# Performance work log

Measured on AMD Instinct MI355X. Metric: run time of the kernel, lower is better.

The kernel has to match this reference:

```python
import math
import jax, jax.numpy as jnp
import numpy as np

N, C, T, V = 32, 256, 128, 25
DK, DV, NH = 64, 256, 8
DKH, DVH = DK // NH, DV // NH
EPS = 1e-5


def _spatial_pe(channels, joints):
    # spatial positional encoding: position = joint index, same for all frames
    pos = jnp.arange(joints, dtype=jnp.float32)  # (V,)
    div = jnp.exp(jnp.arange(0, channels, 2, dtype=jnp.float32) * (-math.log(10000.0) / channels))
    ang = pos[:, None] * div[None, :]  # (V, C/2)
    pe = jnp.stack([jnp.sin(ang), jnp.cos(ang)], axis=-1).reshape(joints, channels)  # interleave sin/cos
    return pe.T  # (C, V)


def _qkv_heads(inp, qkv_w, qkv_b):
    # inp: (N, T, C, V); 1x1 conv == channel GEMM
    qkv = jnp.einsum('oc,ntcv->ntov', qkv_w, inp) + qkv_b[None, None, :, None]
    q = qkv[:, :, :DK].reshape(N, T, NH, DKH, V) * (DKH ** -0.5)
    k = qkv[:, :, DK:2 * DK].reshape(N, T, NH, DKH, V)
    g = qkv[:, :, 2 * DK:3 * DK].reshape(N, T, NH, DKH, V)
    v = qkv[:, :, 3 * DK:].reshape(N, T, NH, DVH, V)
    return q, k, g, v


def setup_inputs() -> dict:
    key = jax.random.key(0)
    ks = jax.random.split(key, 3)
    return {
        'x': jax.random.normal(ks[0], (N, C, T, V), dtype=jnp.float32),
        'qkv_w': jax.random.normal(ks[1], (3 * DK + DV, C), dtype=jnp.float32) * 0.02,
        'qkv_b': jnp.zeros((3 * DK + DV,), dtype=jnp.float32),
        'attn_w': jax.random.normal(ks[2], (DV, DV), dtype=jnp.float32) * 0.02,
        'attn_b': jnp.zeros((DV,), dtype=jnp.float32),
        'dbn_gamma': jnp.ones((C * V,), dtype=jnp.float32),
        'dbn_beta': jnp.zeros((C * V,), dtype=jnp.float32),
        'bn_gamma': jnp.ones((DV,), dtype=jnp.float32),
        'bn_beta': jnp.zeros((DV,), dtype=jnp.float32),
    }


def reference(x, qkv_w, qkv_b, attn_w, attn_b, dbn_gamma, dbn_beta, bn_gamma, bn_beta):
    x_sum = x
    pe = _spatial_pe(C, V)  # (C, V)
    pos = x + pe[None, :, None, :]  # broadcast over N, T

    # data_bn: BatchNorm1d over C*V features (training mode, batch stats over N and T)
    xr = x.transpose(0, 1, 3, 2).reshape(N, C * V, T)
    mu = xr.mean(axis=(0, 2))
    var = xr.var(axis=(0, 2))
    xr = (xr - mu[None, :, None]) * jax.lax.rsqrt(var + EPS)[None, :, None]
    xr = xr * dbn_gamma[None, :, None] + dbn_beta[None, :, None]
    xn = xr.reshape(N, C, V, T).transpose(0, 1, 3, 2)  # (N, C, T, V)

    xa = xn.transpose(0, 2, 1, 3)   # (N, T, C, V)
    pa = pos.transpose(0, 2, 1, 3)  # (N, T, C, V)

    q, k, g, v = _qkv_heads(xa, qkv_w, qkv_b)
    pq, pk, _, _ = _qkv_heads(pa, qkv_w, qkv_b)

    mu_q = q.mean(-1, keepdims=True)          # (N,T,Nh,dkh,1)
    qc = q - mu_q
    pairwise = jnp.einsum('nthdv,nthdw->nthvw', qc, k)    # (N,T,Nh,V,V)
    unary = jnp.einsum('nthdv,nthdw->nthvw', mu_q, g)     # (N,T,Nh,1,V)
    lp = jnp.einsum('nthdv,nthdw->nthvw', pq, pk)         # (N,T,Nh,V,V)

    weights = jnp.tanh(pairwise + lp) + jnp.tanh(unary + lp)
    attn = jnp.einsum('nthvw,nthew->nthev', weights, v)   # (N,T,Nh,dvh,V)
    attn = attn.reshape(N, T, DV, V)
    attn = jnp.einsum('oe,ntev->ntov', attn_w, attn) + attn_b[None, None, :, None]
    y = attn.transpose(0, 2, 1, 3) + x_sum  # skip (in_c == out_c)

    # bn: BatchNorm2d over out_c (training mode)
    mu2 = y.mean(axis=(0, 2, 3))
    var2 = y.var(axis=(0, 2, 3))
    y = (y - mu2[None, :, None, None]) * jax.lax.rsqrt(var2 + EPS)[None, :, None, None]
    y = y * bn_gamma[None, :, None, None] + bn_beta[None, :, None, None]
    return jax.nn.relu(y)
```

## Files before the change

kernel.cpp:

```cpp
#include <hip/hip_runtime.h>
#include <hip/hip_bf16.h>
#include <math.h>

#define N_   32
#define C_   256
#define T_   128
#define V_   25
#define CTV  (C_ * T_ * V_)
#define TV   (T_ * V_)
#define EPS_ 1e-5f
#define S_Q  0.35355339059327373f
#define NCOPY 64

typedef __attribute__((ext_vector_type(8))) short bf16x8;
typedef __attribute__((ext_vector_type(4))) float f32x4;

__device__ inline ushort f2b(float f) {
    __hip_bfloat16 h = __float2bfloat16(f);
    return *reinterpret_cast<ushort*>(&h);
}
__device__ inline float b2f(ushort u) {
    __hip_bfloat16 h;
    *reinterpret_cast<ushort*>(&h) = u;
    return __bfloat162float(h);
}
__device__ inline float tanh_fast(float x) {
    float xc = fminf(fmaxf(x, -12.f), 12.f);
    float e = __expf(xc + xc);
    return (e - 1.f) * __builtin_amdgcn_rcpf(e + 1.f);
}
#define LD8(p) (*(const bf16x8*)(p))
#define MFMA16(a, b, c) __builtin_amdgcn_mfma_f32_16x16x32_bf16(a, b, c, 0, 0, 0)

__device__ inline int qtswz(int v, int col) {
    return v * 320 + ((((col >> 3)) ^ (v & 7)) << 3) + (col & 7);
}
__device__ inline int qvswz(int e, int w) {
    return e * 32 + (((w >> 3) ^ (e & 3)) << 3) + (w & 7);
}
__device__ inline int bswz(int v, int c) {
    return v * 256 + ((((c >> 3) ^ (v & 7)) << 3) | (c & 7));
}

__global__ void prep_kernel(const float* __restrict__ qkv_w,
                            const float* __restrict__ attn_w,
                            ushort* __restrict__ Wq, ushort* __restrict__ Wa,
                            float* __restrict__ pe, float* __restrict__ bins) {
    int idx = blockIdx.x * blockDim.x + threadIdx.x;
    int stride = gridDim.x * blockDim.x;
    for (int i = idx; i < 448 * 256; i += stride) {
        float w = qkv_w[i];
        if (i < 64 * 256) w *= S_Q;
        Wq[i] = f2b(w);
    }
    for (int i = idx; i < 256 * 256; i += stride) Wa[i] = f2b(attn_w[i]);
    for (int i = idx; i < C_ * V_; i += stride) {
        int c = i / V_, v = i - c * V_;
        int j2 = c & ~1;
        float ang = (float)v * expf(-logf(10000.0f) * (float)j2 / (float)C_);
        pe[i] = (c & 1) ? cosf(ang) : sinf(ang);
    }
    for (int i = idx; i < NCOPY * 512; i += stride) bins[i] = 0.f;
}

__global__ __launch_bounds__(1024) void dbn_kernel(const float* __restrict__ x,
                                                   const float* __restrict__ gamma,
                                                   const float* __restrict__ beta,
                                                   float* __restrict__ a_scale,
                                                   float* __restrict__ a_shift) {
    __shared__ float pgS[32][25], pgQ[32][25];
    int c = blockIdx.x;
    int tid = threadIdx.x, g = tid >> 5, l = tid & 31;
    float s = 0.f, s2 = 0.f;
    if (l < 25) {
        const float* base = x + (size_t)g * CTV + c * TV + l;
        #pragma unroll 8
        for (int t = 0; t < 128; ++t) {
            float v = base[t * 25];
            s += v; s2 += v * v;
        }
        pgS[g][l] = s; pgQ[g][l] = s2;
    }
    __syncthreads();
    if (tid < 25) {
        float S = 0.f, Q = 0.f;
        #pragma unroll
        for (int g2 = 0; g2 < 32; ++g2) { S += pgS[g2][tid]; Q += pgQ[g2][tid]; }
        float inv = 1.0f / 4096.0f;
        float mean = S * inv, var = Q * inv - mean * mean;
        int f = c * 25 + tid;
        float sc = rsqrtf(var + EPS_) * gamma[f];
        a_scale[f] = sc;
        a_shift[f] = beta[f] - mean * sc;
    }
}

__global__ void mkbias_kernel(const ushort* __restrict__ Wq,
                              const float* __restrict__ qkv_b,
                              const float* __restrict__ a_shift,
                              const float* __restrict__ pe,
                              float* __restrict__ bias2, float* __restrict__ peproj) {
    int id = blockIdx.x * 256 + threadIdx.x;
    if (id < 11200) {
        int o = id / 25, v = id - o * 25;
        float acc = qkv_b[o] * (o < 64 ? S_Q : 1.f);
        for (int c = 0; c < 256; ++c)
            acc = fmaf(b2f(Wq[o * 256 + c]), a_shift[c * 25 + v], acc);
        bias2[id] = acc;
    } else if (id < 14400) {
        int id2 = id - 11200;
        int r = id2 / 25, v = id2 - r * 25;
        float acc = qkv_b[r] * (r < 64 ? S_Q : 1.f);
        for (int c = 0; c < 256; ++c)
            acc = fmaf(b2f(Wq[r * 256 + c]), pe[c * 25 + v], acc);
        peproj[id2] = acc;
    }
}

__global__ __launch_bounds__(512, 4) void fused_kernel(
        const float* __restrict__ x,
        const ushort* __restrict__ Wq,
        const float* __restrict__ bias2, const float* __restrict__ peproj,
        const float* __restrict__ a_scale,
        const ushort* __restrict__ Wa, const float* __restrict__ attn_b,
        float* __restrict__ out, float* __restrict__ bins) {
    __shared__ __align__(16) char smem[53248];
    ushort* Braw = (ushort*)smem;
    ushort* Bxn  = (ushort*)(smem + 16384);
    ushort* qkvT = (ushort*)(smem + 32768);
    ushort* qkvV = (ushort*)smem;
    ushort* aT   = (ushort*)(smem + 16384);
    ushort* pbuf = (ushort*)(smem + 32768);

    int n = blockIdx.x >> 7, t = blockIdx.x & 127;
    int tid = threadIdx.x, wave = tid >> 6, lane = tid & 63;
    int lr = lane & 15, lg = lane >> 4;
    const float* xp = x + (size_t)n * CTV + t * V_;
    float* outp = out + (size_t)n * CTV + t * V_;
    float* mybins = bins + (blockIdx.x & (NCOPY - 1)) * 512;
    const f32x4 zacc = {0.f, 0.f, 0.f, 0.f};
    const bf16x8 zero8 = {0, 0, 0, 0, 0, 0, 0, 0};

    for (int i = tid; i < 6400; i += 512) {
        int c = i / 25, v = i - c * 25;
        float xv = xp[c * TV + v];
        int off = bswz(v, c);
        Braw[off] = f2b(xv);
        Bxn[off]  = f2b(xv * a_scale[i]);
    }
    for (int i = tid; i < 1792; i += 512) {
        int v = 25 + (i >> 8), c = i & 255;
        int off = v * 256 + c;
        Braw[off] = 0; Bxn[off] = 0;
    }
    __syncthreads();

    {
        const ushort* Arow = Wq + (wave * 16 + lr) * 256;
        f32x4 a0 = zacc, a1 = zacc;
        #pragma unroll
        for (int kk = 0; kk < 8; ++kk) {
            int k0 = kk * 32 + lg * 8;
            int oct = (((k0 >> 3) ^ (lr & 7)) << 3);
            bf16x8 a  = LD8(Arow + k0);
            bf16x8 b0 = LD8(Braw + lr * 256 + oct);
            bf16x8 b1 = LD8(Braw + (16 + lr) * 256 + oct);
            a0 = MFMA16(a, b0, a0);
            a1 = MFMA16(a, b1, a1);
        }
        #pragma unroll
        for (int i2 = 0; i2 < 4; ++i2) {
            int r = wave * 16 + lg * 4 + i2;
            qkvT[qtswz(lr, 192 + r)] = f2b(a0[i2] + peproj[r * 25 + lr]);
            qkvT[qtswz(16 + lr, 192 + r)] =
                (lr < 9) ? f2b(a1[i2] + peproj[r * 25 + 16 + lr]) : (ushort)0;
        }
    }
    __syncthreads();

    {
        int myTiles = (wave < 4) ? 4 : 3;
        f32x4 acc[4][2];
        #pragma unroll
        for (int i = 0; i < 4; ++i) { acc[i][0] = zacc; acc[i][1] = zacc; }
        #pragma unroll
        for (int kk = 0; kk < 8; ++kk) {
            int k0 = kk * 32 + lg * 8;
            int oct = (((k0 >> 3) ^ (lr & 7)) << 3);
            bf16x8 b0 = LD8(Bxn + lr * 256 + oct);
            bf16x8 b1 = LD8(Bxn + (16 + lr) * 256 + oct);
            #pragma unroll
            for (int tt = 0; tt < 4; ++tt) {
                if (tt < myTiles) {
                    int mt = wave + tt * 8;
                    bf16x8 a = LD8(Wq + (mt * 16 + lr) * 256 + k0);
                    acc[tt][0] = MFMA16(a, b0, acc[tt][0]);
                    acc[tt][1] = MFMA16(a, b1, acc[tt][1]);
                }
            }
        }
        #pragma unroll
        for (int tt = 0; tt < 4; ++tt) {
            if (tt < myTiles) {
                int mt = wave + tt * 8;
                #pragma unroll
                for (int i2 = 0; i2 < 4; ++i2) {
                    int o = mt * 16 + lg * 4 + i2;
                    float v0 = acc[tt][0][i2] + bias2[o * 25 + lr];
                    float v1 = acc[tt][1][i2] + ((lr < 9) ? bias2[o * 25 + 16 + lr] : 0.f);
                    if (mt < 12) {
                        qkvT[qtswz(lr, o)] = f2b(v0);
                        qkvT[qtswz(16 + lr, o)] = (lr < 9) ? f2b(v1) : (ushort)0;
                    } else {
                        int e = o - 192;
                        qkvV[qvswz(e, lr)] = f2b(v0);
                        qkvV[qvswz(e, 16 + lr)] = (lr < 9) ? f2b(v1) : (ushort)0;
                    }
                }
            }
        }
    }
    __syncthreads();

    int h = wave;
    float qs = 0.f;
    if (lane < 8) {
        #pragma unroll
        for (int v = 0; v < 25; ++v)
            qs += b2f(qkvT[v * 320 + ((h ^ (v & 7)) << 3) + lane]);
        qs *= (1.f / 25.f);
    }
    float m[8];
    #pragma unroll
    for (int d = 0; d < 8; ++d) m[d] = __shfl(qs, d, 64);
    float u1a = 0.f, u1b = 0.f, u2a = 0.f, u2b = 0.f;
    {
        int ra = lr, rb = 16 + lr;
        int ka = ((8 + h) ^ (ra & 7)) << 3, kb = ((8 + h) ^ (rb & 7)) << 3;
        int ga = ((16 + h) ^ (ra & 7)) << 3, gb = ((16 + h) ^ (rb & 7)) << 3;
        #pragma unroll
        for (int d = 0; d < 8; ++d) {
            u1a = fmaf(m[d], b2f(qkvT[ra * 320 + ka + d]), u1a);
            u1b = fmaf(m[d], b2f(qkvT[rb * 320 + kb + d]), u1b);
            u2a = fmaf(m[d], b2f(qkvT[ra * 320 + ga + d]), u2a);
            u2b = fmaf(m[d], b2f(qkvT[rb * 320 + gb + d]), u2b);
        }
    }
    bf16x8 aP1[2], aP2[2], bP1[2], bP2[2];
    #pragma unroll
    for (int mi = 0; mi < 2; ++mi) {
        int row = mi * 16 + lr, sx = row & 7;
        const ushort* rp = qkvT + row * 320;
        aP1[mi] = (lg == 0) ? LD8(rp + ((h ^ sx) << 3))
                : (lg == 1) ? LD8(rp + (((24 + h) ^ sx) << 3)) : zero8;
        aP2[mi] = (lg == 0) ? LD8(rp + (((24 + h) ^ sx) << 3)) : zero8;
        bP1[mi] = (lg == 0) ? LD8(rp + (((8 + h) ^ sx) << 3))
                : (lg == 1) ? LD8(rp + (((32 + h) ^ sx) << 3)) : zero8;
        bP2[mi] = (lg == 0) ? LD8(rp + (((32 + h) ^ sx) << 3)) : zero8;
    }
    f32x4 p1[2][2], p2[2][2];
    #pragma unroll
    for (int mi = 0; mi < 2; ++mi)
        #pragma unroll
        for (int ni = 0; ni < 2; ++ni) {
            p1[mi][ni] = MFMA16(aP1[mi], bP1[ni], zacc);
            p2[mi][ni] = MFMA16(aP2[mi], bP2[ni], zacc);
        }
    __syncthreads();

    #pragma unroll
    for (int mi = 0; mi < 2; ++mi)
        #pragma unroll
        for (int ni = 0; ni < 2; ++ni) {
            float uu1 = ni ? u1b : u1a, uu2 = ni ? u2b : u2a;
            int w = ni * 16 + lr;
            #pragma unroll
            for (int i2 = 0; i2 < 4; ++i2) {
                int v = mi * 16 + lg * 4 + i2;
                float tw = tanh_fast(p1[mi][ni][i2] - uu1) + tanh_fast(p2[mi][ni][i2] + uu2);
                pbuf[(h * 32 + v) * 40 + w] = (w < 25) ? f2b(tw) : (ushort)0;
            }
        }

    {
        bf16x8 aw[2], bv[2];
        #pragma unroll
        for (int mi = 0; mi < 2; ++mi)
            aw[mi] = LD8(pbuf + (h * 32 + mi * 16 + lr) * 40 + lg * 8);
        #pragma unroll
        for (int ni = 0; ni < 2; ++ni) {
            int e = h * 32 + ni * 16 + lr;
            bv[ni] = LD8(qkvV + e * 32 + ((lg ^ (e & 3)) << 3));
        }
        f32x4 at_[2][2];
        #pragma unroll
        for (int mi = 0; mi < 2; ++mi)
            #pragma unroll
            for (int ni = 0; ni < 2; ++ni)
                at_[mi][ni] = MFMA16(aw[mi], bv[ni], zacc);
        #pragma unroll
        for (int mi = 0; mi < 2; ++mi)
            #pragma unroll
            for (int ni = 0; ni < 2; ++ni)
                #pragma unroll
                for (int i2 = 0; i2 < 4; ++i2) {
                    int v = mi * 16 + lg * 4 + i2;
                    int e = h * 32 + ni * 16 + lr;
                    aT[bswz(v, e)] = (v < 25) ? f2b(at_[mi][ni][i2]) : (ushort)0;
                }
    }
    __syncthreads();

    #pragma unroll
    for (int tt = 0; tt < 2; ++tt) {
        int o0 = (wave + tt * 8) * 16;
        const ushort* Arow = Wa + (o0 + lr) * 256;
        f32x4 a0 = zacc, a1 = zacc;
        #pragma unroll
        for (int kk = 0; kk < 8; ++kk) {
            int k0 = kk * 32 + lg * 8;
            int oct = (((k0 >> 3) ^ (lr & 7)) << 3);
            bf16x8 a  = LD8(Arow + k0);
            bf16x8 b0 = LD8(aT + lr * 256 + oct);
            bf16x8 b1 = LD8(aT + (16 + lr) * 256 + oct);
            a0 = MFMA16(a, b0, a0);
            a1 = MFMA16(a, b1, a1);
        }
        #pragma unroll
        for (int i2 = 0; i2 < 4; ++i2) {
            int o = o0 + lg * 4 + i2;
            float bias = attn_b[o];
            float v0 = a0[i2] + bias + xp[o * TV + lr];
            outp[o * TV + lr] = v0;
            float v1 = 0.f;
            if (lr < 9) {
                v1 = a1[i2] + bias + xp[o * TV + 16 + lr];
                outp[o * TV + 16 + lr] = v1;
            }
            float cs = v0 + v1, cq = v0 * v0 + v1 * v1;
            #pragma unroll
            for (int mm = 1; mm < 16; mm <<= 1) {
                cs += __shfl_xor(cs, mm, 64);
                cq += __shfl_xor(cq, mm, 64);
            }
            if (lr == 0) {
                atomicAdd(&mybins[o], cs);
                atomicAdd(&mybins[256 + o], cq);
            }
        }
    }
}

__global__ void bn2_final_kernel(const float* __restrict__ bins,
                                 const float* __restrict__ gamma,
                                 const float* __restrict__ beta,
                                 float* __restrict__ scale,
                                 float* __restrict__ shift) {
    int c = threadIdx.x;
    float s = 0.f, q = 0.f;
    for (int cp = 0; cp < NCOPY; ++cp) {
        s += bins[cp * 512 + c];
        q += bins[cp * 512 + 256 + c];
    }
    float inv = 1.0f / (float)(N_ * TV);
    float mean = s * inv;
    float var = q * inv - mean * mean;
    float sc = rsqrtf(var + EPS_) * gamma[c];
    scale[c] = sc;
    shift[c] = beta[c] - mean * sc;
}

__global__ void bn2_apply_kernel(float4* __restrict__ y,
                                 const float* __restrict__ scale,
                                 const float* __restrict__ shift) {
    const int total4 = N_ * CTV / 4;
    for (int i = blockIdx.x * blockDim.x + threadIdx.x; i < total4;
         i += gridDim.x * blockDim.x) {
        int c = (i / (TV / 4)) & 255;
        float4 v = y[i];
        float sc = scale[c], sh = shift[c];
        v.x = fmaxf(fmaf(v.x, sc, sh), 0.f);
        v.y = fmaxf(fmaf(v.y, sc, sh), 0.f);
        v.z = fmaxf(fmaf(v.z, sc, sh), 0.f);
        v.w = fmaxf(fmaf(v.w, sc, sh), 0.f);
        y[i] = v;
    }
}

extern "C" void kernel_launch(void* const* d_in, const int* in_sizes, int n_in,
                              void* d_out, int out_size, void* d_ws, size_t ws_size,
                              hipStream_t stream) {
    const float* x      = (const float*)d_in[0];
    const float* qkv_w  = (const float*)d_in[1];
    const float* qkv_b  = (const float*)d_in[2];
    const float* attn_w = (const float*)d_in[3];
    const float* attn_b = (const float*)d_in[4];
    const float* dbn_g  = (const float*)d_in[5];
    const float* dbn_b  = (const float*)d_in[6];
    const float* bn_g   = (const float*)d_in[7];
    const float* bn_b   = (const float*)d_in[8];
    float* out = (float*)d_out;

    char* ws = (char*)d_ws;
    ushort* Wq      = (ushort*)ws;
    ushort* Wa      = (ushort*)(ws + 229376);
    float*  pe      = (float*)(ws + 360448);
    float*  a_scale = (float*)(ws + 386048);
    float*  a_shift = (float*)(ws + 411648);
    float*  bias2   = (float*)(ws + 437248);
    float*  peproj  = (float*)(ws + 482048);
    float*  bins    = (float*)(ws + 494848);
    float*  bn2_sc  = (float*)(ws + 625920);
    float*  bn2_sh  = (float*)(ws + 626944);

    prep_kernel<<<256, 256, 0, stream>>>(qkv_w, attn_w, Wq, Wa, pe, bins);
    dbn_kernel<<<C_, 1024, 0, stream>>>(x, dbn_g, dbn_b, a_scale, a_shift);
    mkbias_kernel<<<57, 256, 0, stream>>>(Wq, qkv_b, a_shift, pe, bias2, peproj);
    fused_kernel<<<N_ * T_, 512, 0, stream>>>(x, Wq, bias2, peproj, a_scale,
                                              Wa, attn_b, out, bins);
    bn2_final_kernel<<<1, 256, 0, stream>>>(bins, bn_g, bn_b, bn2_sc, bn2_sh);
    bn2_apply_kernel<<<4096, 256, 0, stream>>>((float4*)out, bn2_sc, bn2_sh);
}
```

Before: 380.3 us.

## Fold query-mean centering and unary term into MFMA via K-extension

Computes the per-head query mean inside the QKV GEMM epilogue through a shuffle reduction plus a precomputed bias sum. The centered q is stored directly, and the mean and g vectors are packed as extra K lanes of the second pairwise MFMA, so the separate scalar mean and unary loops disappear. It also prefetches x and the scale into registers before the LDS stores, vectorizes the LDS stores, and preloads the skip-connection values before the output GEMM. This adds a tiny extra kernel and a small LDS region. Rounding the mean to bf16 slightly changes the numerics.

```diff
diff --git a/kernel.cpp b/kernel.cpp
--- a/kernel.cpp
+++ b/kernel.cpp
@@ -14,6 +14,7 @@
 
 typedef __attribute__((ext_vector_type(8))) short bf16x8;
 typedef __attribute__((ext_vector_type(4))) float f32x4;
+typedef __attribute__((ext_vector_type(4))) unsigned short u16x4;
 
 __device__ inline ushort f2b(float f) {
     __hip_bfloat16 h = __float2bfloat16(f);
@@ -117,20 +118,30 @@
     }
 }
 
+__global__ void b2sum_kernel(const float* __restrict__ bias2,
+                             float* __restrict__ bias2sum) {
+    int o = threadIdx.x;
+    float s = 0.f;
+    #pragma unroll
+    for (int v = 0; v < 25; ++v) s += bias2[o * 25 + v];
+    bias2sum[o] = s;
+}
+
 __global__ __launch_bounds__(512, 4) void fused_kernel(
         const float* __restrict__ x,
         const ushort* __restrict__ Wq,
         const float* __restrict__ bias2, const float* __restrict__ peproj,
-        const float* __restrict__ a_scale,
+        const float* __restrict__ a_scale, const float* __restrict__ bias2sum,
         const ushort* __restrict__ Wa, const float* __restrict__ attn_b,
         float* __restrict__ out, float* __restrict__ bins) {
-    __shared__ __align__(16) char smem[53248];
+    __shared__ __align__(16) char smem[53376];
     ushort* Braw = (ushort*)smem;
     ushort* Bxn  = (ushort*)(smem + 16384);
     ushort* qkvT = (ushort*)(smem + 32768);
     ushort* qkvV = (ushort*)smem;
     ushort* aT   = (ushort*)(smem + 16384);
     ushort* pbuf = (ushort*)(smem + 32768);
+    ushort* qmub = (ushort*)(smem + 53248);
 
     int n = blockIdx.x >> 7, t = blockIdx.x & 127;
     int tid = threadIdx.x, wave = tid >> 6, lane = tid & 63;
@@ -141,17 +152,40 @@
     const f32x4 zacc = {0.f, 0.f, 0.f, 0.f};
     const bf16x8 zero8 = {0, 0, 0, 0, 0, 0, 0, 0};
 
-    for (int i = tid; i < 6400; i += 512) {
-        int c = i / 25, v = i - c * 25;
-        float xv = xp[c * TV + v];
-        int off = bswz(v, c);
-        Braw[off] = f2b(xv);
-        Bxn[off]  = f2b(xv * a_scale[i]);
-    }
-    for (int i = tid; i < 1792; i += 512) {
-        int v = 25 + (i >> 8), c = i & 255;
-        int off = v * 256 + c;
-        Braw[off] = 0; Bxn[off] = 0;
+    float b2s[4] = {0.f, 0.f, 0.f, 0.f};
+    if (wave < 4) {
+        #pragma unroll
+        for (int i2 = 0; i2 < 4; ++i2)
+            b2s[i2] = bias2sum[wave * 16 + lg * 4 + i2];
+    }
+
+    {
+        float xv[13], sc[13];
+        #pragma unroll
+        for (int j = 0; j < 13; ++j) {
+            int i = tid + j * 512;
+            if (i < 6400) {
+                int c = i / 25, v = i - c * 25;
+                xv[j] = xp[c * TV + v];
+                sc[j] = a_scale[i];
+            }
+        }
+        #pragma unroll
+        for (int j = 0; j < 13; ++j) {
+            int i = tid + j * 512;
+            if (i < 6400) {
+                int c = i / 25, v = i - c * 25;
+                int off = bswz(v, c);
+                Braw[off] = f2b(xv[j]);
+                Bxn[off]  = f2b(xv[j] * sc[j]);
+            }
+        }
+        for (int i = tid; i < 448; i += 512) {
+            int v = 25 + (i >> 6), c = (i & 63) * 4;
+            u16x4 z4 = {0, 0, 0, 0};
+            *(u16x4*)(Braw + v * 256 + c) = z4;
+            *(u16x4*)(Bxn + v * 256 + c) = z4;
+        }
     }
     __syncthreads();
 
@@ -168,13 +202,16 @@
             a0 = MFMA16(a, b0, a0);
             a1 = MFMA16(a, b1, a1);
         }
+        int rb = wave * 16 + lg * 4;
+        u16x4 r0, r1;
         #pragma unroll
         for (int i2 = 0; i2 < 4; ++i2) {
-            int r = wave * 16 + lg * 4 + i2;
-            qkvT[qtswz(lr, 192 + r)] = f2b(a0[i2] + peproj[r * 25 + lr]);
-            qkvT[qtswz(16 + lr, 192 + r)] =
-                (lr < 9) ? f2b(a1[i2] + peproj[r * 25 + 16 + lr]) : (ushort)0;
-        }
+            int r = rb + i2;
+            r0[i2] = f2b(a0[i2] + peproj[r * 25 + lr]);
+            r1[i2] = (lr < 9) ? f2b(a1[i2] + peproj[r * 25 + 16 + lr]) : (ushort)0;
+        }
+        *(u16x4*)(qkvT + qtswz(lr, 192 + rb)) = r0;
+        *(u16x4*)(qkvT + qtswz(16 + lr, 192 + rb)) = r1;
     }
     __syncthreads();
 
@@ -203,18 +240,48 @@
         for (int tt = 0; tt < 4; ++tt) {
             if (tt < myTiles) {
                 int mt = wave + tt * 8;
-                #pragma unroll
-                for (int i2 = 0; i2 < 4; ++i2) {
-                    int o = mt * 16 + lg * 4 + i2;
-                    float v0 = acc[tt][0][i2] + bias2[o * 25 + lr];
-                    float v1 = acc[tt][1][i2] + ((lr < 9) ? bias2[o * 25 + 16 + lr] : 0.f);
-                    if (mt < 12) {
-                        qkvT[qtswz(lr, o)] = f2b(v0);
-                        qkvT[qtswz(16 + lr, o)] = (lr < 9) ? f2b(v1) : (ushort)0;
-                    } else {
+                int ob = mt * 16 + lg * 4;
+                if (mt < 4) {
+                    u16x4 r0, r1;
+                    #pragma unroll
+                    for (int i2 = 0; i2 < 4; ++i2) {
+                        int o = ob + i2;
+                        float cs = acc[tt][0][i2] + ((lr < 9) ? acc[tt][1][i2] : 0.f);
+                        #pragma unroll
+                        for (int mm = 1; mm < 16; mm <<= 1)
+                            cs += __shfl_xor(cs, mm, 64);
+                        float mu = (cs + b2s[i2]) * 0.04f;
+                        ushort mur = f2b(mu);
+                        float muf = b2f(mur);
+                        r0[i2] = f2b(acc[tt][0][i2] + bias2[o * 25 + lr] - muf);
+                        r1[i2] = (lr < 9)
+                            ? f2b(acc[tt][1][i2] + bias2[o * 25 + 16 + lr] - muf)
+                            : (ushort)0;
+                        if (lr == 0) qmub[o] = mur;
+                    }
+                    *(u16x4*)(qkvT + qtswz(lr, ob)) = r0;
+                    *(u16x4*)(qkvT + qtswz(16 + lr, ob)) = r1;
+                } else if (mt < 12) {
+                    u16x4 r0, r1;
+                    #pragma unroll
+                    for (int i2 = 0; i2 < 4; ++i2) {
+                        int o = ob + i2;
+                        r0[i2] = f2b(acc[tt][0][i2] + bias2[o * 25 + lr]);
+                        r1[i2] = (lr < 9)
+                            ? f2b(acc[tt][1][i2] + bias2[o * 25 + 16 + lr])
+                            : (ushort)0;
+                    }
+                    *(u16x4*)(qkvT + qtswz(lr, ob)) = r0;
+                    *(u16x4*)(qkvT + qtswz(16 + lr, ob)) = r1;
+                } else {
+                    #pragma unroll
+                    for (int i2 = 0; i2 < 4; ++i2) {
+                        int o = ob + i2;
                         int e = o - 192;
-                        qkvV[qvswz(e, lr)] = f2b(v0);
-                        qkvV[qvswz(e, 16 + lr)] = (lr < 9) ? f2b(v1) : (ushort)0;
+                        qkvV[qvswz(e, lr)] = f2b(acc[tt][0][i2] + bias2[o * 25 + lr]);
+                        qkvV[qvswz(e, 16 + lr)] = (lr < 9)
+                            ? f2b(acc[tt][1][i2] + bias2[o * 25 + 16 + lr])
+                            : (ushort)0;
                     }
                 }
             }
@@ -223,29 +290,7 @@
     __syncthreads();
 
     int h = wave;
-    float qs = 0.f;
-    if (lane < 8) {
-        #pragma unroll
-        for (int v = 0; v < 25; ++v)
-            qs += b2f(qkvT[v * 320 + ((h ^ (v & 7)) << 3) + lane]);
-        qs *= (1.f / 25.f);
-    }
-    float m[8];
-    #pragma unroll
-    for (int d = 0; d < 8; ++d) m[d] = __shfl(qs, d, 64);
-    float u1a = 0.f, u1b = 0.f, u2a = 0.f, u2b = 0.f;
-    {
-        int ra = lr, rb = 16 + lr;
-        int ka = ((8 + h) ^ (ra & 7)) << 3, kb = ((8 + h) ^ (rb & 7)) << 3;
-        int ga = ((16 + h) ^ (ra & 7)) << 3, gb = ((16 + h) ^ (rb & 7)) << 3;
-        #pragma unroll
-        for (int d = 0; d < 8; ++d) {
-            u1a = fmaf(m[d], b2f(qkvT[ra * 320 + ka + d]), u1a);
-            u1b = fmaf(m[d], b2f(qkvT[rb * 320 + kb + d]), u1b);
-            u2a = fmaf(m[d], b2f(qkvT[ra * 320 + ga + d]), u2a);
-            u2b = fmaf(m[d], b2f(qkvT[rb * 320 + gb + d]), u2b);
-        }
-    }
+    bf16x8 mu8 = LD8(qmub + h * 8);
     bf16x8 aP1[2], aP2[2], bP1[2], bP2[2];
     #pragma unroll
     for (int mi = 0; mi < 2; ++mi) {
@@ -253,10 +298,12 @@
         const ushort* rp = qkvT + row * 320;
         aP1[mi] = (lg == 0) ? LD8(rp + ((h ^ sx) << 3))
                 : (lg == 1) ? LD8(rp + (((24 + h) ^ sx) << 3)) : zero8;
-        aP2[mi] = (lg == 0) ? LD8(rp + (((24 + h) ^ sx) << 3)) : zero8;
+        aP2[mi] = (lg == 0) ? LD8(rp + (((24 + h) ^ sx) << 3))
+                : (lg == 1) ? mu8 : zero8;
         bP1[mi] = (lg == 0) ? LD8(rp + (((8 + h) ^ sx) << 3))
                 : (lg == 1) ? LD8(rp + (((32 + h) ^ sx) << 3)) : zero8;
-        bP2[mi] = (lg == 0) ? LD8(rp + (((32 + h) ^ sx) << 3)) : zero8;
+        bP2[mi] = (lg == 0) ? LD8(rp + (((32 + h) ^ sx) << 3))
+                : (lg == 1) ? LD8(rp + (((16 + h) ^ sx) << 3)) : zero8;
     }
     f32x4 p1[2][2], p2[2][2];
     #pragma unroll
@@ -272,12 +319,11 @@
     for (int mi = 0; mi < 2; ++mi)
         #pragma unroll
         for (int ni = 0; ni < 2; ++ni) {
-            float uu1 = ni ? u1b : u1a, uu2 = ni ? u2b : u2a;
             int w = ni * 16 + lr;
             #pragma unroll
             for (int i2 = 0; i2 < 4; ++i2) {
                 int v = mi * 16 + lg * 4 + i2;
-                float tw = tanh_fast(p1[mi][ni][i2] - uu1) + tanh_fast(p2[mi][ni][i2] + uu2);
+                float tw = tanh_fast(p1[mi][ni][i2]) + tanh_fast(p2[mi][ni][i2]);
                 pbuf[(h * 32 + v) * 40 + w] = (w < 25) ? f2b(tw) : (ushort)0;
             }
         }
@@ -306,11 +352,20 @@
                 for (int i2 = 0; i2 < 4; ++i2) {
                     int v = mi * 16 + lg * 4 + i2;
                     int e = h * 32 + ni * 16 + lr;
-                    aT[bswz(v, e)] = (v < 25) ? f2b(at_[mi][ni][i2]) : (ushort)0;
+                    if (v < 25) aT[bswz(v, e)] = f2b(at_[mi][ni][i2]);
                 }
     }
     __syncthreads();
 
+    float sk0[2][4], sk1[2][4];
+    #pragma unroll
+    for (int tt = 0; tt < 2; ++tt)
+        #pragma unroll
+        for (int i2 = 0; i2 < 4; ++i2) {
+            int o = (wave + tt * 8) * 16 + lg * 4 + i2;
+            sk0[tt][i2] = xp[o * TV + lr];
+            sk1[tt][i2] = (lr < 9) ? xp[o * TV + 16 + lr] : 0.f;
+        }
     #pragma unroll
     for (int tt = 0; tt < 2; ++tt) {
         int o0 = (wave + tt * 8) * 16;
@@ -330,11 +385,11 @@
         for (int i2 = 0; i2 < 4; ++i2) {
             int o = o0 + lg * 4 + i2;
             float bias = attn_b[o];
-            float v0 = a0[i2] + bias + xp[o * TV + lr];
+            float v0 = a0[i2] + bias + sk0[tt][i2];
             outp[o * TV + lr] = v0;
             float v1 = 0.f;
             if (lr < 9) {
-                v1 = a1[i2] + bias + xp[o * TV + 16 + lr];
+                v1 = a1[i2] + bias + sk1[tt][i2];
                 outp[o * TV + 16 + lr] = v1;
             }
             float cs = v0 + v1, cq = v0 * v0 + v1 * v1;
@@ -402,22 +457,24 @@
     float* out = (float*)d_out;
 
     char* ws = (char*)d_ws;
-    ushort* Wq      = (ushort*)ws;
-    ushort* Wa      = (ushort*)(ws + 229376);
-    float*  pe      = (float*)(ws + 360448);
-    float*  a_scale = (float*)(ws + 386048);
-    float*  a_shift = (float*)(ws + 411648);
-    float*  bias2   = (float*)(ws + 437248);
-    float*  peproj  = (float*)(ws + 482048);
-    float*  bins    = (float*)(ws + 494848);
-    float*  bn2_sc  = (float*)(ws + 625920);
-    float*  bn2_sh  = (float*)(ws + 626944);
+    ushort* Wq       = (ushort*)ws;
+    ushort* Wa       = (ushort*)(ws + 229376);
+    float*  pe       = (float*)(ws + 360448);
+    float*  a_scale  = (float*)(ws + 386048);
+    float*  a_shift  = (float*)(ws + 411648);
+    float*  bias2    = (float*)(ws + 437248);
+    float*  peproj   = (float*)(ws + 482048);
+    float*  bias2sum = (float*)(ws + 494848);
+    float*  bins     = (float*)(ws + 495104);
+    float*  bn2_sc   = (float*)(ws + 626176);
+    float*  bn2_sh   = (float*)(ws + 627200);
 
     prep_kernel<<<256, 256, 0, stream>>>(qkv_w, attn_w, Wq, Wa, pe, bins);
     dbn_kernel<<<C_, 1024, 0, stream>>>(x, dbn_g, dbn_b, a_scale, a_shift);
     mkbias_kernel<<<57, 256, 0, stream>>>(Wq, qkv_b, a_shift, pe, bias2, peproj);
+    b2sum_kernel<<<1, 64, 0, stream>>>(bias2, bias2sum);
     fused_kernel<<<N_ * T_, 512, 0, stream>>>(x, Wq, bias2, peproj, a_scale,
-                                              Wa, attn_b, out, bins);
+                                              bias2sum, Wa, attn_b, out, bins);
     bn2_final_kernel<<<1, 256, 0, stream>>>(bins, bn_g, bn_b, bn2_sc, bn2_sh);
     bn2_apply_kernel<<<4096, 256, 0, stream>>>((float4*)out, bn2_sc, bn2_sh);
 }
```

After: 352.8 us. -7.2%, faster.
